# Kernel optimization log

Measured on AMD Instinct MI355X. Metric: run time of the kernel, lower is better.

## Reference

```python
import jax, jax.numpy as jnp
import numpy as np

B, S, E, H, F = 32, 512, 1024, 8, 8192
D = E // H  # head_dim = 128


def setup_inputs() -> dict:
    key = jax.random.key(0)
    ks = jax.random.split(key, 6)
    w = 0.02  # init scale
    return {
        "x": jax.random.normal(ks[0], (B, S, E), dtype=jnp.float32),
        "Wq": jax.random.normal(ks[1], (E, E), dtype=jnp.float32) * w,
        "bq": jnp.zeros((E,), dtype=jnp.float32),
        "Wk": jax.random.normal(ks[2], (E, E), dtype=jnp.float32) * w,
        "bk": jnp.zeros((E,), dtype=jnp.float32),
        "Wv": jax.random.normal(ks[3], (E, E), dtype=jnp.float32) * w,
        "bv": jnp.zeros((E,), dtype=jnp.float32),
        "W1": jax.random.normal(ks[4], (E, F), dtype=jnp.float32) * w,
        "b1": jnp.zeros((F,), dtype=jnp.float32),
        "W2": jax.random.normal(ks[5], (F, E), dtype=jnp.float32) * w,
        "b2": jnp.zeros((E,), dtype=jnp.float32),
    }


def reference(x, Wq, bq, Wk, bk, Wv, bv, W1, b1, W2, b2):
    b, s, e = x.shape
    h, d = H, e // H
    # headed projections: [b, h, s, d]
    q = (x @ Wq + bq).reshape(b, s, h, d).transpose(0, 2, 1, 3)
    k = (x @ Wk + bk).reshape(b, s, h, d).transpose(0, 2, 1, 3)
    v = (x @ Wv + bv).reshape(b, s, h, d).transpose(0, 2, 1, 3)
    # NOTE: original applies NO 1/sqrt(d) scaling
    scores = jnp.einsum("bhqd,bhkd->bhqk", q, k)
    attn = jax.nn.softmax(scores, axis=-1)
    o = jnp.einsum("bhqk,bhkd->bhqd", attn, v)
    o = o.transpose(0, 2, 1, 3).reshape(b, s, e)  # concat heads
    hid = jax.nn.gelu(o @ W1 + b1, approximate=False)  # nn.GELU default = exact erf
    return hid @ W2 + b2
```

## Files before the change

### kernel.cpp

```cpp
#include <hip/hip_runtime.h>
#include <hip/hip_bf16.h>
#include <math.h>

typedef __attribute__((ext_vector_type(8))) short bf16x8;
typedef __attribute__((ext_vector_type(4))) float f32x4;
typedef __hip_bfloat16 bf16;

__device__ __forceinline__ void gload_lds16(const void* g, void* l) {
  __builtin_amdgcn_global_load_lds((const __attribute__((address_space(1))) void*)g,
                                   (__attribute__((address_space(3))) void*)l,
                                   16, 0, 0);
}

__device__ __forceinline__ float gelu_erf(float x) {
  return 0.5f * x * (1.0f + erff(x * 0.70710678118654752f));
}

__global__ __launch_bounds__(256) void k_cvt_bf16(const float* __restrict__ in,
                                                  bf16* __restrict__ out, int n4) {
  int i = blockIdx.x * 256 + threadIdx.x;
  const int stride = gridDim.x * 256;
  for (; i < n4; i += stride) {
    float4 v = reinterpret_cast<const float4*>(in)[i];
    bf16* o = out + (size_t)i * 4;
    o[0] = __float2bfloat16(v.x);
    o[1] = __float2bfloat16(v.y);
    o[2] = __float2bfloat16(v.z);
    o[3] = __float2bfloat16(v.w);
  }
}

__global__ __launch_bounds__(256) void k_transpose_w(const float* __restrict__ in,
                                                     bf16* __restrict__ out,
                                                     int R, int C) {
  __shared__ float tile[32][33];
  const int c0 = blockIdx.x * 32, r0 = blockIdx.y * 32;
  const int tx = threadIdx.x & 31, ty = threadIdx.x >> 5;
  for (int i = 0; i < 32; i += 8)
    tile[ty + i][tx] = in[(size_t)(r0 + ty + i) * C + c0 + tx];
  __syncthreads();
  for (int i = 0; i < 32; i += 8)
    out[(size_t)(c0 + ty + i) * R + r0 + tx] = __float2bfloat16(tile[tx][ty + i]);
}

__global__ __launch_bounds__(256) void k_transpose_v(const bf16* __restrict__ Vb,
                                                     bf16* __restrict__ Vt) {
  __shared__ bf16 tile[32][34];
  const int bh = blockIdx.z;
  const int b = bh >> 3, h = bh & 7;
  const int s0 = blockIdx.x * 32, d0 = blockIdx.y * 32;
  const int tx = threadIdx.x & 31, ty = threadIdx.x >> 5;
  for (int i = 0; i < 32; i += 8)
    tile[ty + i][tx] = Vb[((size_t)b * 512 + s0 + ty + i) * 1024 + h * 128 + d0 + tx];
  __syncthreads();
  for (int i = 0; i < 32; i += 8)
    Vt[((size_t)bh * 128 + d0 + ty + i) * 512 + s0 + tx] = tile[tx][ty + i];
}

template <int EPI, bool ACC>
__global__ __launch_bounds__(512, 2) void k_gemm256(
    const bf16* __restrict__ A, const bf16* __restrict__ Bt,
    const float* __restrict__ bias, void* __restrict__ Cout,
    int K, int lda, int ldb, int ldc) {
  __shared__ __attribute__((aligned(16))) char lds[131072];
  const int t = threadIdx.x, w = t >> 6, l = t & 63;
  const int gx = gridDim.x, nwg = gx * gridDim.y;
  int bid = blockIdx.y * gx + blockIdx.x;
  bid = (bid & 7) * (nwg >> 3) + (bid >> 3);
  const int bm = bid / gx, bn = bid % gx;
  const int wm = w >> 2, wn = w & 3;
  const int lq = l >> 4, lr = l & 15;

  const int srow = (w << 3) + (l >> 3);
  const int scol = ((l & 7) ^ ((l >> 3) & 7)) << 4;
  const size_t ldab = (size_t)lda * 2, ldbb = (size_t)ldb * 2;
  const size_t ldab64 = ldab * 64, ldbb64 = ldbb * 64;
  const char* pA = (const char*)(A + (size_t)(bm * 256) * lda) + (size_t)srow * ldab + scol;
  const char* pB = (const char*)(Bt + (size_t)(bn * 256) * ldb) + (size_t)srow * ldbb + scol;
  const int ldst = w * 1024;

  const int swz0 = (lq ^ (lr & 7)) << 4;
  const int arow = wm * 16384 + lr * 128;
  const int brow = 32768 + (wn >> 1) * 16384 + ((wn & 1) * 64 + lr) * 128;

  f32x4 acc[8][4];
#pragma unroll
  for (int m = 0; m < 8; ++m)
#pragma unroll
    for (int n = 0; n < 4; ++n) acc[m][n] = (f32x4){0.f, 0.f, 0.f, 0.f};

#define STAGE_A(j, slotbase)                                            \
  gload_lds16(pA + (size_t)(j)*ldab64, (slotbase) + (j)*8192 + ldst)
#define STAGE_B(j, slotbase)                                            \
  gload_lds16(pB + (size_t)(j)*ldbb64, (slotbase) + 32768 + (j)*8192 + ldst)

  {
    char* s0 = lds;
    STAGE_A(0, s0); STAGE_A(1, s0); STAGE_A(2, s0); STAGE_A(3, s0);
    STAGE_B(0, s0); STAGE_B(1, s0); STAGE_B(2, s0); STAGE_B(3, s0);
    pA += 128; pB += 128;
    asm volatile("s_waitcnt vmcnt(0)" ::: "memory");
    __builtin_amdgcn_s_barrier();
    asm volatile("" ::: "memory");
  }

  const int NT = K >> 6;
  bf16x8 aF[4][2], bF01[2][2], bF23[2][2];

  for (int kt = 0; kt < NT; ++kt) {
    char* cur = lds + (kt & 1) * 65536;
    char* nxt = lds + ((kt & 1) ^ 1) * 65536;
    const char* Ac = cur + arow;
    const char* Bc = cur + brow;
    const bool pre = (kt + 1 < NT);

#pragma unroll
    for (int fr = 0; fr < 4; ++fr)
#pragma unroll
      for (int kk = 0; kk < 2; ++kk)
        aF[fr][kk] = *(const bf16x8*)(Ac + fr * 2048 + (swz0 ^ (kk << 6)));
#pragma unroll
    for (int fc = 0; fc < 2; ++fc)
#pragma unroll
      for (int kk = 0; kk < 2; ++kk)
        bF01[fc][kk] = *(const bf16x8*)(Bc + fc * 2048 + (swz0 ^ (kk << 6)));
    if (pre) { STAGE_A(0, nxt); STAGE_A(1, nxt); STAGE_A(2, nxt); STAGE_A(3, nxt); }
    __builtin_amdgcn_s_barrier();
    __builtin_amdgcn_s_setprio(1);
#pragma unroll
    for (int fr = 0; fr < 4; ++fr)
#pragma unroll
      for (int fc = 0; fc < 2; ++fc)
#pragma unroll
        for (int kk = 0; kk < 2; ++kk)
          acc[fr][fc] = __builtin_amdgcn_mfma_f32_16x16x32_bf16(aF[fr][kk], bF01[fc][kk], acc[fr][fc], 0, 0, 0);
    __builtin_amdgcn_s_setprio(0);
    __builtin_amdgcn_s_barrier();

#pragma unroll
    for (int fc = 0; fc < 2; ++fc)
#pragma unroll
      for (int kk = 0; kk < 2; ++kk)
        bF23[fc][kk] = *(const bf16x8*)(Bc + (2 + fc) * 2048 + (swz0 ^ (kk << 6)));
    if (pre) { STAGE_B(0, nxt); STAGE_B(1, nxt); }
    __builtin_amdgcn_s_barrier();
    __builtin_amdgcn_s_setprio(1);
#pragma unroll
    for (int fr = 0; fr < 4; ++fr)
#pragma unroll
      for (int fc = 0; fc < 2; ++fc)
#pragma unroll
        for (int kk = 0; kk < 2; ++kk)
          acc[fr][2 + fc] = __builtin_amdgcn_mfma_f32_16x16x32_bf16(aF[fr][kk], bF23[fc][kk], acc[fr][2 + fc], 0, 0, 0);
    __builtin_amdgcn_s_setprio(0);
    __builtin_amdgcn_s_barrier();

#pragma unroll
    for (int fr = 0; fr < 4; ++fr)
#pragma unroll
      for (int kk = 0; kk < 2; ++kk)
        aF[fr][kk] = *(const bf16x8*)(Ac + (4 + fr) * 2048 + (swz0 ^ (kk << 6)));
    if (pre) { STAGE_B(2, nxt); STAGE_B(3, nxt); }
    __builtin_amdgcn_s_barrier();
    __builtin_amdgcn_s_setprio(1);
#pragma unroll
    for (int fr = 0; fr < 4; ++fr)
#pragma unroll
      for (int fc = 0; fc < 2; ++fc)
#pragma unroll
        for (int kk = 0; kk < 2; ++kk)
          acc[4 + fr][fc] = __builtin_amdgcn_mfma_f32_16x16x32_bf16(aF[fr][kk], bF01[fc][kk], acc[4 + fr][fc], 0, 0, 0);
    __builtin_amdgcn_s_setprio(0);
    __builtin_amdgcn_s_barrier();

    __builtin_amdgcn_s_setprio(1);
#pragma unroll
    for (int fr = 0; fr < 4; ++fr)
#pragma unroll
      for (int fc = 0; fc < 2; ++fc)
#pragma unroll
        for (int kk = 0; kk < 2; ++kk)
          acc[4 + fr][2 + fc] = __builtin_amdgcn_mfma_f32_16x16x32_bf16(aF[fr][kk], bF23[fc][kk], acc[4 + fr][2 + fc], 0, 0, 0);
    __builtin_amdgcn_s_setprio(0);
    asm volatile("s_waitcnt vmcnt(0)" ::: "memory");
    __builtin_amdgcn_s_barrier();
    asm volatile("" ::: "memory");

    if (pre) { pA += 128; pB += 128; }
  }
#undef STAGE_A
#undef STAGE_B

  const int rowb = bm * 256 + wm * 128;
  const int colb = bn * 256 + wn * 64;
#pragma unroll
  for (int fr = 0; fr < 8; ++fr) {
#pragma unroll
    for (int fc = 0; fc < 4; ++fc) {
      const int col = colb + fc * 16 + lr;
      const float bv = bias ? bias[col] : 0.0f;
#pragma unroll
      for (int i = 0; i < 4; ++i) {
        const int row = rowb + fr * 16 + lq * 4 + i;
        float v = acc[fr][fc][i] + bv;
        if (EPI == 1) v = gelu_erf(v);
        if (EPI <= 1) {
          ((bf16*)Cout)[(size_t)row * ldc + col] = __float2bfloat16(v);
        } else {
          float* Cf = (float*)Cout;
          const size_t idx = (size_t)row * ldc + col;
          if (ACC) v += Cf[idx];
          Cf[idx] = v;
        }
      }
    }
  }
}

__global__ __launch_bounds__(512, 1) void k_attn(const bf16* __restrict__ Qg,
                                                 const bf16* __restrict__ Kg,
                                                 const bf16* __restrict__ Vt,
                                                 bf16* __restrict__ Og) {
  __shared__ __attribute__((aligned(16))) char lds[131072];
  int bid = blockIdx.x;
  bid = (bid & 7) * 128 + (bid >> 3);
  const int bh = bid >> 2, q0 = (bid & 3) * 128;
  const int b = bh >> 3, h = bh & 7;
  const int t = threadIdx.x, w = t >> 6, l = t & 63;
  const int lq = l >> 4, lr = l & 15;
  const int wm = w >> 2, wn = w & 3;

  const int sr = t >> 4;
  const int ss = (t & 15) ^ (sr & 15);
  {
    const bf16* ks = Kg + ((size_t)b * 512 + sr) * 1024 + h * 128 + ss * 8;
#pragma unroll
    for (int j = 0; j < 16; ++j)
      gload_lds16(ks + (size_t)j * 32 * 1024, lds + j * 8192 + w * 1024);
  }

  bf16x8 qf[4][4];
  {
    const bf16* qb = Qg + ((size_t)b * 512 + q0 + wm * 64 + lr) * 1024 + h * 128 + lq * 8;
#pragma unroll
    for (int fr = 0; fr < 4; ++fr)
#pragma unroll
      for (int d0 = 0; d0 < 4; ++d0)
        qf[fr][d0] = *(const bf16x8*)(qb + (size_t)(fr * 16) * 1024 + d0 * 32);
  }

  asm volatile("s_waitcnt vmcnt(0)" ::: "memory");
  __builtin_amdgcn_s_barrier();
  asm volatile("" ::: "memory");

  f32x4 accS[4][8];
#pragma unroll
  for (int fr = 0; fr < 4; ++fr)
#pragma unroll
    for (int fc = 0; fc < 8; ++fc) accS[fr][fc] = (f32x4){0.f, 0.f, 0.f, 0.f};

  __builtin_amdgcn_s_setprio(1);
#pragma unroll
  for (int fc = 0; fc < 8; ++fc) {
    bf16x8 kf[4];
#pragma unroll
    for (int d0 = 0; d0 < 4; ++d0)
      kf[d0] = *(const bf16x8*)(lds + (wn * 128 + fc * 16 + lr) * 256 +
                                (((d0 * 4 + lq) ^ lr) << 4));
#pragma unroll
    for (int d0 = 0; d0 < 4; ++d0)
#pragma unroll
      for (int fr = 0; fr < 4; ++fr)
        accS[fr][fc] = __builtin_amdgcn_mfma_f32_16x16x32_bf16(qf[fr][d0], kf[d0], accS[fr][fc], 0, 0, 0);
  }
  __builtin_amdgcn_s_setprio(0);

  __builtin_amdgcn_s_barrier();
  asm volatile("" ::: "memory");

  const bf16* vs = Vt + ((size_t)bh * 128 + sr) * 512 + ss * 8;
#define IVC(kc, slot)                                                         \
  {                                                                           \
    _Pragma("unroll") for (int j = 0; j < 4; ++j)                             \
        gload_lds16(vs + (size_t)j * 32 * 512 + (kc) * 128,                   \
                    lds + (slot) * 32768 + j * 8192 + w * 1024);              \
  }
  IVC(0, 0)
  IVC(1, 1)

  float* redm = (float*)(lds + 98304);
  float* reds = (float*)(lds + 100352);
  float fm[4][4];
#pragma unroll
  for (int fr = 0; fr < 4; ++fr)
#pragma unroll
    for (int i = 0; i < 4; ++i) {
      float m = accS[fr][0][i];
#pragma unroll
      for (int fc = 1; fc < 8; ++fc) m = fmaxf(m, accS[fr][fc][i]);
      m = fmaxf(m, __shfl_xor(m, 1));
      m = fmaxf(m, __shfl_xor(m, 2));
      m = fmaxf(m, __shfl_xor(m, 4));
      m = fmaxf(m, __shfl_xor(m, 8));
      if (lr == 0) redm[wn * 128 + wm * 64 + fr * 16 + lq * 4 + i] = m;
    }
  asm volatile("s_waitcnt lgkmcnt(0)" ::: "memory");
  __builtin_amdgcn_s_barrier();
  asm volatile("" ::: "memory");
#pragma unroll
  for (int fr = 0; fr < 4; ++fr)
#pragma unroll
    for (int i = 0; i < 4; ++i) {
      const int row = wm * 64 + fr * 16 + lq * 4 + i;
      fm[fr][i] = fmaxf(fmaxf(redm[row], redm[128 + row]),
                        fmaxf(redm[256 + row], redm[384 + row]));
    }

  f32x4 oacc[4][2];
#pragma unroll
  for (int fr = 0; fr < 4; ++fr)
#pragma unroll
    for (int fc = 0; fc < 2; ++fc) oacc[fr][fc] = (f32x4){0.f, 0.f, 0.f, 0.f};
  float s4[4][4];
#pragma unroll
  for (int fr = 0; fr < 4; ++fr)
#pragma unroll
    for (int i = 0; i < 4; ++i) s4[fr][i] = 0.f;

#define EXPWRITE(kc)                                                           \
  if (wn == (kc)) {                                                            \
    _Pragma("unroll") for (int fr = 0; fr < 4; ++fr)                           \
      _Pragma("unroll") for (int i = 0; i < 4; ++i) {                          \
        const int row = wm * 64 + fr * 16 + lq * 4 + i;                        \
        const int rx = lq * 4 + i;                                             \
        _Pragma("unroll") for (int fc = 0; fc < 8; ++fc) {                     \
          const float e = __expf(accS[fr][fc][i] - fm[fr][i]);                 \
          s4[fr][i] += e;                                                      \
          *(unsigned short*)(lds + 65536 + row * 256 +                         \
                             (((fc * 2 + (lr >> 3)) ^ rx) << 4) + (lr & 7) * 2) = \
              __bfloat16_as_ushort(__float2bfloat16(e));                       \
        }                                                                      \
      }                                                                        \
  }

#define PVMFMA(kc)                                                             \
  {                                                                            \
    const char* Vb = lds + ((kc) & 1) * 32768;                                 \
    __builtin_amdgcn_s_setprio(1);                                             \
    _Pragma("unroll") for (int kk = 0; kk < 4; ++kk) {                         \
      bf16x8 pa[4], vb[2];                                                     \
      _Pragma("unroll") for (int fr = 0; fr < 4; ++fr)                         \
          pa[fr] = *(const bf16x8*)(lds + 65536 + (wm * 64 + fr * 16 + lr) * 256 + \
                                    (((kk * 4 + lq) ^ lr) << 4));              \
      _Pragma("unroll") for (int fc = 0; fc < 2; ++fc)                         \
          vb[fc] = *(const bf16x8*)(Vb + (wn * 32 + fc * 16 + lr) * 256 +      \
                                    (((kk * 4 + lq) ^ lr) << 4));              \
      _Pragma("unroll") for (int fr = 0; fr < 4; ++fr)                         \
        _Pragma("unroll") for (int fc = 0; fc < 2; ++fc)                       \
          oacc[fr][fc] = __builtin_amdgcn_mfma_f32_16x16x32_bf16(pa[fr], vb[fc], oacc[fr][fc], 0, 0, 0); \
    }                                                                          \
    __builtin_amdgcn_s_setprio(0);                                             \
  }

  EXPWRITE(0)
  asm volatile("s_waitcnt lgkmcnt(0)" ::: "memory");
  asm volatile("s_waitcnt vmcnt(4)" ::: "memory");
  __builtin_amdgcn_s_barrier();
  asm volatile("" ::: "memory");
  PVMFMA(0)
  __builtin_amdgcn_s_barrier();
  asm volatile("" ::: "memory");
  IVC(2, 0)
  EXPWRITE(1)
  asm volatile("s_waitcnt lgkmcnt(0)" ::: "memory");
  asm volatile("s_waitcnt vmcnt(4)" ::: "memory");
  __builtin_amdgcn_s_barrier();
  asm volatile("" ::: "memory");
  PVMFMA(1)
  __builtin_amdgcn_s_barrier();
  asm volatile("" ::: "memory");
  IVC(3, 1)
  EXPWRITE(2)
  asm volatile("s_waitcnt lgkmcnt(0)" ::: "memory");
  asm volatile("s_waitcnt vmcnt(4)" ::: "memory");
  __builtin_amdgcn_s_barrier();
  asm volatile("" ::: "memory");
  PVMFMA(2)
  __builtin_amdgcn_s_barrier();
  asm volatile("" ::: "memory");
  EXPWRITE(3)
  asm volatile("s_waitcnt lgkmcnt(0)" ::: "memory");
  asm volatile("s_waitcnt vmcnt(0)" ::: "memory");
  __builtin_amdgcn_s_barrier();
  asm volatile("" ::: "memory");
  PVMFMA(3)
#undef IVC
#undef EXPWRITE
#undef PVMFMA

#pragma unroll
  for (int fr = 0; fr < 4; ++fr)
#pragma unroll
    for (int i = 0; i < 4; ++i) {
      float s = s4[fr][i];
      s += __shfl_xor(s, 1);
      s += __shfl_xor(s, 2);
      s += __shfl_xor(s, 4);
      s += __shfl_xor(s, 8);
      if (lr == 0) reds[wn * 128 + wm * 64 + fr * 16 + lq * 4 + i] = s;
    }
  asm volatile("s_waitcnt lgkmcnt(0)" ::: "memory");
  __builtin_amdgcn_s_barrier();
  asm volatile("" ::: "memory");

#pragma unroll
  for (int fr = 0; fr < 4; ++fr)
#pragma unroll
    for (int i = 0; i < 4; ++i) {
      const int row = wm * 64 + fr * 16 + lq * 4 + i;
      const float rs = (reds[row] + reds[128 + row]) + (reds[256 + row] + reds[384 + row]);
#pragma unroll
      for (int fc = 0; fc < 2; ++fc) {
        const int col = wn * 32 + fc * 16 + lr;
        Og[((size_t)b * 512 + q0 + row) * 1024 + h * 128 + col] =
            __float2bfloat16(oacc[fr][fc][i] / rs);
      }
    }
}

extern "C" void kernel_launch(void* const* d_in, const int* in_sizes, int n_in,
                              void* d_out, int out_size, void* d_ws, size_t ws_size,
                              hipStream_t stream) {
  (void)in_sizes; (void)n_in; (void)out_size; (void)ws_size;
  const float* x  = (const float*)d_in[0];
  const float* Wq = (const float*)d_in[1];
  const float* bq = (const float*)d_in[2];
  const float* Wk = (const float*)d_in[3];
  const float* bk = (const float*)d_in[4];
  const float* Wv = (const float*)d_in[5];
  const float* bv = (const float*)d_in[6];
  const float* W1 = (const float*)d_in[7];
  const float* b1 = (const float*)d_in[8];
  const float* W2 = (const float*)d_in[9];
  const float* b2 = (const float*)d_in[10];
  float* out = (float*)d_out;
  char* ws = (char*)d_ws;
  constexpr size_t MB = 1ull << 20;

  bf16* XB  = (bf16*)(ws + 0);
  bf16* WQT = (bf16*)(ws + 32 * MB);
  bf16* WKT = (bf16*)(ws + 34 * MB);
  bf16* WVT = (bf16*)(ws + 36 * MB);
  bf16* W1T = (bf16*)(ws + 38 * MB);
  bf16* W2T = (bf16*)(ws + 54 * MB);
  bf16* OB  = (bf16*)(ws + 70 * MB);
  bf16* QB  = (bf16*)(ws + 102 * MB);
  bf16* KB  = (bf16*)(ws + 134 * MB);
  bf16* VB  = (bf16*)(ws + 166 * MB);
  bf16* VT  = (bf16*)(ws + 0);
  bf16* HC  = (bf16*)(ws + 102 * MB);

  k_cvt_bf16<<<2048, 256, 0, stream>>>(x, XB, (16384 * 1024) / 4);
  k_transpose_w<<<dim3(32, 32), 256, 0, stream>>>(Wq, WQT, 1024, 1024);
  k_transpose_w<<<dim3(32, 32), 256, 0, stream>>>(Wk, WKT, 1024, 1024);
  k_transpose_w<<<dim3(32, 32), 256, 0, stream>>>(Wv, WVT, 1024, 1024);
  k_transpose_w<<<dim3(256, 32), 256, 0, stream>>>(W1, W1T, 1024, 8192);
  k_transpose_w<<<dim3(32, 256), 256, 0, stream>>>(W2, W2T, 8192, 1024);

  k_gemm256<0, false><<<dim3(4, 64), 512, 0, stream>>>(XB, WQT, bq, QB, 1024, 1024, 1024, 1024);
  k_gemm256<0, false><<<dim3(4, 64), 512, 0, stream>>>(XB, WKT, bk, KB, 1024, 1024, 1024, 1024);
  k_gemm256<0, false><<<dim3(4, 64), 512, 0, stream>>>(XB, WVT, bv, VB, 1024, 1024, 1024, 1024);

  k_transpose_v<<<dim3(16, 4, 256), 256, 0, stream>>>(VB, VT);
  k_attn<<<1024, 512, 0, stream>>>(QB, KB, VT, OB);

  for (int chk = 0; chk < 4; ++chk) {
    k_gemm256<1, false><<<dim3(8, 64), 512, 0, stream>>>(
        OB, W1T + (size_t)chk * 2048 * 1024, b1 + chk * 2048, HC, 1024, 1024, 1024, 2048);
    if (chk == 0)
      k_gemm256<2, false><<<dim3(4, 64), 512, 0, stream>>>(
          HC, W2T + chk * 2048, b2, out, 2048, 2048, 8192, 1024);
    else
      k_gemm256<2, true><<<dim3(4, 64), 512, 0, stream>>>(
          HC, W2T + chk * 2048, nullptr, out, 2048, 2048, 8192, 1024);
  }
}
```

Baseline: 987.0 us.

## Split GEMM tile loads into quarter-stages with partial vmcnt waits

Reorganises the 256x256 GEMM main loop so the A and B tiles are each loaded as two halves, laid out in LDS by the sub-block each wave quadrant consumes. Waits use partial vmcnt counts instead of draining all loads at the end of every K-step. Next-tile loads can therefore overlap with MFMA work across iterations. This adds complex wait-count bookkeeping, and a miscount could read data before it has landed.

```diff
diff --git a/kernel.cpp b/kernel.cpp
--- a/kernel.cpp
+++ b/kernel.cpp
@@ -71,17 +71,23 @@
   const int wm = w >> 2, wn = w & 3;
   const int lq = l >> 4, lr = l & 15;
 
-  const int srow = (w << 3) + (l >> 3);
-  const int scol = ((l & 7) ^ ((l >> 3) & 7)) << 4;
-  const size_t ldab = (size_t)lda * 2, ldbb = (size_t)ldb * 2;
-  const size_t ldab64 = ldab * 64, ldbb64 = ldbb * 64;
-  const char* pA = (const char*)(A + (size_t)(bm * 256) * lda) + (size_t)srow * ldab + scol;
-  const char* pB = (const char*)(Bt + (size_t)(bn * 256) * ldb) + (size_t)srow * ldbb + scol;
-  const int ldst = w * 1024;
-
-  const int swz0 = (lq ^ (lr & 7)) << 4;
-  const int arow = wm * 16384 + lr * 128;
-  const int brow = 32768 + (wn >> 1) * 16384 + ((wn & 1) * 64 + lr) * 128;
+  const char* Ab = (const char*)(A + (size_t)(bm * 256) * lda);
+  const char* Bb = (const char*)(Bt + (size_t)(bn * 256) * ldb);
+  const int r0 = t >> 3, s0x = ((t & 7) ^ (r0 & 7)) << 4;
+  const int r1 = (t + 512) >> 3, s1x = (((t + 512) & 7) ^ (r1 & 7)) << 4;
+  const size_t la = (size_t)lda * 2, lb = (size_t)ldb * 2;
+  const char* pA00 = Ab + (size_t)((r0 >> 6) * 128 + (r0 & 63)) * la + s0x;
+  const char* pA10 = Ab + (size_t)((r1 >> 6) * 128 + (r1 & 63)) * la + s1x;
+  const char* pA01 = Ab + (size_t)((r0 >> 6) * 128 + 64 + (r0 & 63)) * la + s0x;
+  const char* pA11 = Ab + (size_t)((r1 >> 6) * 128 + 64 + (r1 & 63)) * la + s1x;
+  const char* pB00 = Bb + (size_t)((r0 >> 5) * 64 + (r0 & 31)) * lb + s0x;
+  const char* pB10 = Bb + (size_t)((r1 >> 5) * 64 + (r1 & 31)) * lb + s1x;
+  const char* pB01 = Bb + (size_t)((r0 >> 5) * 64 + 32 + (r0 & 31)) * lb + s0x;
+  const char* pB11 = Bb + (size_t)((r1 >> 5) * 64 + 32 + (r1 & 31)) * lb + s1x;
+
+  const int swzb = (lq ^ (lr & 7)) << 4;
+  const int aoff = wm * 8192 + lr * 128;
+  const int boff = 32768 + wn * 4096 + lr * 128;
 
   f32x4 acc[8][4];
 #pragma unroll
@@ -89,107 +95,70 @@
 #pragma unroll
     for (int n = 0; n < 4; ++n) acc[m][n] = (f32x4){0.f, 0.f, 0.f, 0.f};
 
-#define STAGE_A(j, slotbase)                                            \
-  gload_lds16(pA + (size_t)(j)*ldab64, (slotbase) + (j)*8192 + ldst)
-#define STAGE_B(j, slotbase)                                            \
-  gload_lds16(pB + (size_t)(j)*ldbb64, (slotbase) + 32768 + (j)*8192 + ldst)
-
-  {
-    char* s0 = lds;
-    STAGE_A(0, s0); STAGE_A(1, s0); STAGE_A(2, s0); STAGE_A(3, s0);
-    STAGE_B(0, s0); STAGE_B(1, s0); STAGE_B(2, s0); STAGE_B(3, s0);
-    pA += 128; pB += 128;
-    asm volatile("s_waitcnt vmcnt(0)" ::: "memory");
-    __builtin_amdgcn_s_barrier();
-    asm volatile("" ::: "memory");
-  }
+#define ISSUE_A0(S) { gload_lds16(pA00, (S) + w * 1024); gload_lds16(pA10, (S) + 8192 + w * 1024); pA00 += 128; pA10 += 128; }
+#define ISSUE_A1(S) { gload_lds16(pA01, (S) + 16384 + w * 1024); gload_lds16(pA11, (S) + 16384 + 8192 + w * 1024); pA01 += 128; pA11 += 128; }
+#define ISSUE_B0(S) { gload_lds16(pB00, (S) + 32768 + w * 1024); gload_lds16(pB10, (S) + 32768 + 8192 + w * 1024); pB00 += 128; pB10 += 128; }
+#define ISSUE_B1(S) { gload_lds16(pB01, (S) + 49152 + w * 1024); gload_lds16(pB11, (S) + 49152 + 8192 + w * 1024); pB01 += 128; pB11 += 128; }
+
+  bf16x8 aF[4][2], bF01[2][2], bF23[2][2];
+#define READ_A03(C) { _Pragma("unroll") for (int fr = 0; fr < 4; ++fr) _Pragma("unroll") for (int kk = 0; kk < 2; ++kk) aF[fr][kk] = *(const bf16x8*)((C) + aoff + fr * 2048 + (swzb ^ (kk << 6))); }
+#define READ_A47(C) { _Pragma("unroll") for (int fr = 0; fr < 4; ++fr) _Pragma("unroll") for (int kk = 0; kk < 2; ++kk) aF[fr][kk] = *(const bf16x8*)((C) + 16384 + aoff + fr * 2048 + (swzb ^ (kk << 6))); }
+#define READ_B01(C) { _Pragma("unroll") for (int fc = 0; fc < 2; ++fc) _Pragma("unroll") for (int kk = 0; kk < 2; ++kk) bF01[fc][kk] = *(const bf16x8*)((C) + boff + fc * 2048 + (swzb ^ (kk << 6))); }
+#define READ_B23(C) { _Pragma("unroll") for (int fc = 0; fc < 2; ++fc) _Pragma("unroll") for (int kk = 0; kk < 2; ++kk) bF23[fc][kk] = *(const bf16x8*)((C) + 16384 + boff + fc * 2048 + (swzb ^ (kk << 6))); }
+
+#define MFMA_Q(ACCR, BFR)                                               \
+  { __builtin_amdgcn_s_setprio(1);                                      \
+    _Pragma("unroll") for (int fr = 0; fr < 4; ++fr)                    \
+      _Pragma("unroll") for (int fc = 0; fc < 2; ++fc)                  \
+        _Pragma("unroll") for (int kk = 0; kk < 2; ++kk)                \
+          acc[ACCR + fr][fc + ((&BFR == &bF23) ? 2 : 0)] =              \
+              __builtin_amdgcn_mfma_f32_16x16x32_bf16(aF[fr][kk], BFR[fc][kk], acc[ACCR + fr][fc + ((&BFR == &bF23) ? 2 : 0)], 0, 0, 0); \
+    __builtin_amdgcn_s_setprio(0); }
+
+  ISSUE_A0(lds); ISSUE_B0(lds); ISSUE_B1(lds); ISSUE_A1(lds);
 
   const int NT = K >> 6;
-  bf16x8 aF[4][2], bF01[2][2], bF23[2][2];
-
   for (int kt = 0; kt < NT; ++kt) {
     char* cur = lds + (kt & 1) * 65536;
     char* nxt = lds + ((kt & 1) ^ 1) * 65536;
-    const char* Ac = cur + arow;
-    const char* Bc = cur + brow;
     const bool pre = (kt + 1 < NT);
 
-#pragma unroll
-    for (int fr = 0; fr < 4; ++fr)
-#pragma unroll
-      for (int kk = 0; kk < 2; ++kk)
-        aF[fr][kk] = *(const bf16x8*)(Ac + fr * 2048 + (swz0 ^ (kk << 6)));
-#pragma unroll
-    for (int fc = 0; fc < 2; ++fc)
-#pragma unroll
-      for (int kk = 0; kk < 2; ++kk)
-        bF01[fc][kk] = *(const bf16x8*)(Bc + fc * 2048 + (swz0 ^ (kk << 6)));
-    if (pre) { STAGE_A(0, nxt); STAGE_A(1, nxt); STAGE_A(2, nxt); STAGE_A(3, nxt); }
-    __builtin_amdgcn_s_barrier();
-    __builtin_amdgcn_s_setprio(1);
-#pragma unroll
-    for (int fr = 0; fr < 4; ++fr)
-#pragma unroll
-      for (int fc = 0; fc < 2; ++fc)
-#pragma unroll
-        for (int kk = 0; kk < 2; ++kk)
-          acc[fr][fc] = __builtin_amdgcn_mfma_f32_16x16x32_bf16(aF[fr][kk], bF01[fc][kk], acc[fr][fc], 0, 0, 0);
-    __builtin_amdgcn_s_setprio(0);
-    __builtin_amdgcn_s_barrier();
-
-#pragma unroll
-    for (int fc = 0; fc < 2; ++fc)
-#pragma unroll
-      for (int kk = 0; kk < 2; ++kk)
-        bF23[fc][kk] = *(const bf16x8*)(Bc + (2 + fc) * 2048 + (swz0 ^ (kk << 6)));
-    if (pre) { STAGE_B(0, nxt); STAGE_B(1, nxt); }
-    __builtin_amdgcn_s_barrier();
-    __builtin_amdgcn_s_setprio(1);
-#pragma unroll
-    for (int fr = 0; fr < 4; ++fr)
-#pragma unroll
-      for (int fc = 0; fc < 2; ++fc)
-#pragma unroll
-        for (int kk = 0; kk < 2; ++kk)
-          acc[fr][2 + fc] = __builtin_amdgcn_mfma_f32_16x16x32_bf16(aF[fr][kk], bF23[fc][kk], acc[fr][2 + fc], 0, 0, 0);
-    __builtin_amdgcn_s_setprio(0);
-    __builtin_amdgcn_s_barrier();
-
-#pragma unroll
-    for (int fr = 0; fr < 4; ++fr)
-#pragma unroll
-      for (int kk = 0; kk < 2; ++kk)
-        aF[fr][kk] = *(const bf16x8*)(Ac + (4 + fr) * 2048 + (swz0 ^ (kk << 6)));
-    if (pre) { STAGE_B(2, nxt); STAGE_B(3, nxt); }
-    __builtin_amdgcn_s_barrier();
-    __builtin_amdgcn_s_setprio(1);
-#pragma unroll
-    for (int fr = 0; fr < 4; ++fr)
-#pragma unroll
-      for (int fc = 0; fc < 2; ++fc)
-#pragma unroll
-        for (int kk = 0; kk < 2; ++kk)
-          acc[4 + fr][fc] = __builtin_amdgcn_mfma_f32_16x16x32_bf16(aF[fr][kk], bF01[fc][kk], acc[4 + fr][fc], 0, 0, 0);
-    __builtin_amdgcn_s_setprio(0);
-    __builtin_amdgcn_s_barrier();
-
-    __builtin_amdgcn_s_setprio(1);
-#pragma unroll
-    for (int fr = 0; fr < 4; ++fr)
-#pragma unroll
-      for (int fc = 0; fc < 2; ++fc)
-#pragma unroll
-        for (int kk = 0; kk < 2; ++kk)
-          acc[4 + fr][2 + fc] = __builtin_amdgcn_mfma_f32_16x16x32_bf16(aF[fr][kk], bF23[fc][kk], acc[4 + fr][2 + fc], 0, 0, 0);
-    __builtin_amdgcn_s_setprio(0);
-    asm volatile("s_waitcnt vmcnt(0)" ::: "memory");
-    __builtin_amdgcn_s_barrier();
-    asm volatile("" ::: "memory");
-
-    if (pre) { pA += 128; pB += 128; }
-  }
-#undef STAGE_A
-#undef STAGE_B
+    asm volatile("s_waitcnt vmcnt(4)" ::: "memory");
+    __builtin_amdgcn_s_barrier();
+    READ_A03(cur); READ_B01(cur);
+    if (pre) ISSUE_A0(nxt);
+    __builtin_amdgcn_s_barrier();
+    MFMA_Q(0, bF01)
+    if (pre) { asm volatile("s_waitcnt vmcnt(4)" ::: "memory"); }
+    else     { asm volatile("s_waitcnt vmcnt(2)" ::: "memory"); }
+    __builtin_amdgcn_s_barrier();
+
+    READ_B23(cur);
+    if (pre) ISSUE_B0(nxt);
+    __builtin_amdgcn_s_barrier();
+    MFMA_Q(0, bF23)
+    if (pre) { asm volatile("s_waitcnt vmcnt(4)" ::: "memory"); }
+    else     { asm volatile("s_waitcnt vmcnt(0)" ::: "memory"); }
+    __builtin_amdgcn_s_barrier();
+
+    READ_A47(cur);
+    if (pre) ISSUE_B1(nxt);
+    __builtin_amdgcn_s_barrier();
+    MFMA_Q(4, bF01)
+    __builtin_amdgcn_s_barrier();
+
+    if (pre) ISSUE_A1(nxt);
+    MFMA_Q(4, bF23)
+  }
+#undef ISSUE_A0
+#undef ISSUE_A1
+#undef ISSUE_B0
+#undef ISSUE_B1
+#undef READ_A03
+#undef READ_A47
+#undef READ_B01
+#undef READ_B23
+#undef MFMA_Q
 
   const int rowb = bm * 256 + wm * 128;
   const int colb = bn * 256 + wn * 64;
```

After: 977.4 us. Within noise of the previous version (-1.0%).
